# Optimization experiments

Measured on AMD Instinct MI355X. Metric: run time of the kernel, lower is better.

## Reference

```python
import jax, jax.numpy as jnp
import numpy as np

D_MODEL = 2048
D_INNER = 2048
N_QK = 32
N_V = 32
D_STATE = 64
D_CONV = 4
CHUNK = 128
CONV_DIM = D_INNER + 2 * N_QK * D_STATE  # 6144
IN_OUT = 2 * D_INNER + 2 * N_QK * D_STATE + N_V  # 8224


def setup_inputs() -> dict:
    key = jax.random.key(0)
    ks = jax.random.split(key, 6)
    u = jax.random.normal(ks[0], (2, 4096, D_MODEL), dtype=jnp.float32)
    W_in = jax.random.normal(ks[1], (IN_OUT, D_MODEL), dtype=jnp.float32) * 0.02
    conv_w = jax.random.normal(ks[2], (CONV_DIM, D_CONV), dtype=jnp.float32) * 0.2
    conv_b = jax.random.normal(ks[3], (CONV_DIM,), dtype=jnp.float32) * 0.02
    D = jnp.ones((N_V,), dtype=jnp.float32)
    z_bias = jnp.zeros((D_INNER,), dtype=jnp.float32)
    W_out = jax.random.normal(ks[4], (D_MODEL, D_INNER), dtype=jnp.float32) * 0.02
    return {"u": u, "W_in": W_in, "conv_w": conv_w, "conv_b": conv_b,
            "D": D, "z_bias": z_bias, "W_out": W_out}


def causal_depthwise_conv(x, w, b):
    # x: [B, L, C]; w: [C, K]; b: [C]. Torch Conv1d(groups=C, padding=K-1)[..., :L]
    B, L, C = x.shape
    K = w.shape[1]
    xp = jnp.pad(x, ((0, 0), (K - 1, 0), (0, 0)))
    y = b[None, None, :]
    for k in range(K):
        y = y + xp[:, k:k + L, :] * w[None, None, :, k]
    return y


def ssd_chunk_scan(x, dt, B, C, chunk):
    # Mamba2 SSD with A = -1 per head.
    # x: [b,l,h,p], dt: [b,l,h] (positive), B,C: [b,l,h,n]
    b, l, h, p = x.shape
    n = B.shape[-1]
    nc = l // chunk
    x = x.reshape(b, nc, chunk, h, p)
    dt = dt.reshape(b, nc, chunk, h)
    B = B.reshape(b, nc, chunk, h, n)
    C = C.reshape(b, nc, chunk, h, n)
    a = -dt                                  # A * dt
    cum = jnp.cumsum(a, axis=2)              # [b,nc,q,h]
    xdt = x * dt[..., None]                  # dt_t * x_t
    # ---- intra-chunk (causal, decay exp(cum_q - cum_k), q >= k) ----
    CB = jnp.einsum('bcqhn,bckhn->bchqk', C, B)
    cumT = jnp.swapaxes(cum, 2, 3)           # [b,nc,h,q]
    diff = cumT[..., :, None] - cumT[..., None, :]   # [b,nc,h,q,k]
    mask = jnp.tril(jnp.ones((chunk, chunk), dtype=bool))
    decay = jnp.exp(jnp.where(mask, diff, -jnp.inf))
    y_intra = jnp.einsum('bchqk,bckhp->bcqhp', CB * decay, xdt)
    # ---- per-chunk final states ----
    state_decay = jnp.exp(cum[:, :, -1:, :] - cum)   # [b,nc,q,h]
    states = jnp.einsum('bckhn,bckhp->bchpn', B * state_decay[..., None], xdt)
    chunk_decay = jnp.exp(cum[:, :, -1, :])          # [b,nc,h]
    # ---- inter-chunk recurrence ----
    def step(carry, inp):
        st, cd = inp  # st [b,h,p,n], cd [b,h]
        new = carry * cd[:, :, None, None] + st
        return new, carry  # emit the state *entering* this chunk
    init = jnp.zeros((b, h, p, n), dtype=x.dtype)
    _, prev = jax.lax.scan(step, init,
                           (jnp.moveaxis(states, 1, 0), jnp.moveaxis(chunk_decay, 1, 0)))
    prev = jnp.moveaxis(prev, 0, 1)                  # [b,nc,h,p,n]
    y_inter = jnp.einsum('bcqhn,bchpn->bcqhp', C * jnp.exp(cum)[..., None], prev)
    return (y_intra + y_inter).reshape(b, l, h, p)


def reference(u, W_in, conv_w, conv_b, D, z_bias, W_out):
    b, l, _ = u.shape  # l divisible by CHUNK (padded_len == l)
    xBCzA = jnp.einsum('bld,od->blo', u, W_in)
    xBC = xBCzA[..., :CONV_DIM]
    z = xBCzA[..., CONV_DIM:CONV_DIM + D_INNER]
    A_log = xBCzA[..., CONV_DIM + D_INNER:]
    xBC = causal_depthwise_conv(xBC, conv_w, conv_b)  # activation = identity
    x = xBC[..., :D_INNER]
    Bm = xBC[..., D_INNER:D_INNER + N_QK * D_STATE]
    Cm = xBC[..., D_INNER + N_QK * D_STATE:]
    x = x.reshape(b, l, N_V, D_INNER // N_V)
    Bm = Bm.reshape(b, l, N_QK, D_STATE)
    Cm = Cm.reshape(b, l, N_QK, D_STATE)
    dt = jax.nn.softplus(A_log)                       # [b,l,h]
    x_scan = x / dt[..., None]
    y = ssd_chunk_scan(x_scan, dt, Bm, Cm, CHUNK)
    y = y + D[None, None, :, None] * x                # Du uses undivided x
    y = y.reshape(b, l, D_INNER)
    out = jnp.einsum('bli,oi->blo', y * jax.nn.silu(z + z_bias), W_out)
    return out
```

## Files before the change

kernel.cpp:

```cpp
#include <hip/hip_runtime.h>
#include <math.h>

#define D_MODEL  2048
#define D_INNER  2048
#define N_QK     32
#define N_V      32
#define D_STATE  64
#define D_CONV   4
#define CHUNK    128
#define CONV_DIM 6144
#define IN_OUT   8224
#define BATCH    2
#define SEQ      4096
#define M_ROWS   (BATCH*SEQ)
#define NCHUNK   (SEQ/CHUNK)

typedef unsigned short bf16_t;
typedef __attribute__((ext_vector_type(4))) float f32x4;
typedef __attribute__((ext_vector_type(8))) short bf16x8;

#define SWZ64(r,c)  ((((r)*64)  + (c)) ^ (((r)&7)<<3))
#define SWZ128(r,c) ((((r)*128) + (c)) ^ (((r)&7)<<3))

__device__ __forceinline__ float b2f(bf16_t u) {
    union { unsigned int i; float f; } w; w.i = ((unsigned int)u) << 16; return w.f;
}
__device__ __forceinline__ bf16_t f2b(float f) {
    unsigned int x = __float_as_uint(f);
    return (bf16_t)((x + 0x7FFFu + ((x >> 16) & 1u)) >> 16);
}
__device__ __forceinline__ void store4b(bf16_t* dst, float4 v) {
    ushort4 u; u.x = f2b(v.x); u.y = f2b(v.y); u.z = f2b(v.z); u.w = f2b(v.w);
    *reinterpret_cast<ushort4*>(dst) = u;
}

__device__ __forceinline__ void gload_lds16(const bf16_t* g, bf16_t* l) {
    __builtin_amdgcn_global_load_lds((const __attribute__((address_space(1))) void*)g,
                                     (__attribute__((address_space(3))) void*)l,
                                     16, 0, 0);
}

__global__ __launch_bounds__(256) void f2b_kernel(const float* __restrict__ in,
                                                  bf16_t* __restrict__ out, long n)
{
    const long i = ((long)blockIdx.x * 256 + threadIdx.x) * 4;
    if (i < n) {
        float4 v = *reinterpret_cast<const float4*>(in + i);
        ushort4 o;
        o.x = f2b(v.x); o.y = f2b(v.y); o.z = f2b(v.z); o.w = f2b(v.w);
        *reinterpret_cast<ushort4*>(out + i) = o;
    }
}

template<int NTB, int K, bool OBF16, int NCOLS>
__global__ __launch_bounds__(512, 2) void gemm256(const bf16_t* __restrict__ A,
                                                  const bf16_t* __restrict__ B,
                                                  void* __restrict__ Cv)
{
    constexpr int BK = 64;
    constexpr int NT = K / BK;
    constexpr bool HASTAIL = (NTB * 256 > NCOLS);
    const long ldc = NCOLS;
    __shared__ bf16_t As[2][256 * BK];
    __shared__ bf16_t Bs[2][256 * BK];

    const int nwg = gridDim.x;
    const int bid = blockIdx.x;
    const int wg  = ((nwg & 7) == 0) ? ((bid & 7) * (nwg >> 3) + (bid >> 3)) : bid;
    const int bm = (wg / NTB) * 256;
    const int bn = (wg % NTB) * 256;

    const int tid  = threadIdx.x;
    const int lane = tid & 63;
    const int wv   = tid >> 6;
    const int wr   = wv >> 2, wc = wv & 3;
    const int l15  = lane & 15, l4 = lane >> 4;

    f32x4 acc[8][4];
    #pragma unroll
    for (int i = 0; i < 8; ++i)
        #pragma unroll
        for (int j = 0; j < 4; ++j) acc[i][j] = (f32x4){0.f, 0.f, 0.f, 0.f};

    const bf16_t* Abase = A + (long)bm * K;

    auto stage = [&](int t, int buf) {
        const bf16_t* Ab = Abase + t * BK;
        #pragma unroll
        for (int it = 0; it < 4; ++it) {
            const int seg = it * 512 + tid;
            const int row = seg >> 3, c16 = seg & 7;
            const int sc = (c16 ^ (row & 7)) * 8;
            gload_lds16(Ab + (long)row * K + sc, &As[buf][seg * 8]);
            int br = bn + row;
            if (HASTAIL) br = min(br, NCOLS - 1);
            gload_lds16(B + (long)br * K + t * BK + sc, &Bs[buf][seg * 8]);
        }
    };

    stage(0, 0);
    asm volatile("s_waitcnt vmcnt(0)" ::: "memory");
    __builtin_amdgcn_s_barrier();

    for (int t = 0; t < NT; ++t) {
        const int cur = t & 1;
        if (t + 1 < NT) stage(t + 1, cur ^ 1);
        bf16x8 bfr[4], af[4];
        #pragma unroll
        for (int ks = 0; ks < 2; ++ks) {
            #pragma unroll
            for (int ni = 0; ni < 4; ++ni) {
                const int row = wc * 64 + ni * 16 + l15;
                const int ch = (ks * 4 + l4) ^ (row & 7);
                bfr[ni] = *reinterpret_cast<const bf16x8*>(&Bs[cur][row * 64 + ch * 8]);
            }
            #pragma unroll
            for (int qm = 0; qm < 2; ++qm) {
                #pragma unroll
                for (int mi = 0; mi < 4; ++mi) {
                    const int row = wr * 128 + qm * 64 + mi * 16 + l15;
                    const int ch = (ks * 4 + l4) ^ (row & 7);
                    af[mi] = *reinterpret_cast<const bf16x8*>(&As[cur][row * 64 + ch * 8]);
                }
                __builtin_amdgcn_s_setprio(1);
                #pragma unroll
                for (int mi = 0; mi < 4; ++mi)
                    #pragma unroll
                    for (int ni = 0; ni < 4; ++ni)
                        acc[qm * 4 + mi][ni] = __builtin_amdgcn_mfma_f32_16x16x32_bf16(
                            af[mi], bfr[ni], acc[qm * 4 + mi][ni], 0, 0, 0);
                __builtin_amdgcn_s_setprio(0);
                if (ks * 2 + qm < 3) __builtin_amdgcn_s_barrier();
            }
        }
        asm volatile("s_waitcnt vmcnt(0)" ::: "memory");
        __builtin_amdgcn_s_barrier();
    }

    #pragma unroll
    for (int mf = 0; mf < 8; ++mf) {
        const long grow0 = bm + wr * 128 + mf * 16 + l4 * 4;
        #pragma unroll
        for (int ni = 0; ni < 4; ++ni) {
            const int gcol = bn + wc * 64 + ni * 16 + l15;
            if (HASTAIL && gcol >= NCOLS) continue;
            #pragma unroll
            for (int j = 0; j < 4; ++j) {
                if (OBF16)
                    ((bf16_t*)Cv)[(grow0 + j) * ldc + gcol] = f2b(acc[mf][ni][j]);
                else
                    ((float*)Cv)[(grow0 + j) * ldc + gcol] = acc[mf][ni][j];
            }
        }
    }
}

__device__ __forceinline__ float4 conv4v(const bf16_t* __restrict__ xb, long m, int l,
                                         int col, const float* __restrict__ cw,
                                         const float* __restrict__ cbv)
{
    float4 acc = *reinterpret_cast<const float4*>(cbv + col);
    float4 wc0 = *reinterpret_cast<const float4*>(cw + (long)col * 4);
    float4 wc1 = *reinterpret_cast<const float4*>(cw + (long)col * 4 + 4);
    float4 wc2 = *reinterpret_cast<const float4*>(cw + (long)col * 4 + 8);
    float4 wc3 = *reinterpret_cast<const float4*>(cw + (long)col * 4 + 12);
    const float t0[4] = {wc0.x, wc0.y, wc0.z, wc0.w};
    const float t1[4] = {wc1.x, wc1.y, wc1.z, wc1.w};
    const float t2[4] = {wc2.x, wc2.y, wc2.z, wc2.w};
    const float t3[4] = {wc3.x, wc3.y, wc3.z, wc3.w};
    #pragma unroll
    for (int tap = 0; tap < 4; ++tap) {
        if (l - 3 + tap < 0) continue;
        const bf16_t* p = xb + (m - 3 + tap) * (long)IN_OUT + col;
        ushort4 v = *reinterpret_cast<const ushort4*>(p);
        acc.x = fmaf(b2f(v.x), t0[tap], acc.x);
        acc.y = fmaf(b2f(v.y), t1[tap], acc.y);
        acc.z = fmaf(b2f(v.z), t2[tap], acc.z);
        acc.w = fmaf(b2f(v.w), t3[tap], acc.w);
    }
    return acc;
}

__global__ __launch_bounds__(256) void ssd_states(const bf16_t* __restrict__ xb,
                                                  const float* __restrict__ cw,
                                                  const float* __restrict__ cbv,
                                                  float* __restrict__ states,
                                                  float* __restrict__ cumbuf,
                                                  float* __restrict__ cdecay)
{
    const int h = blockIdx.x, c = blockIdx.y, b = blockIdx.z;
    __shared__ bf16_t sx [128 * 64];
    __shared__ bf16_t sBr[128 * 64];
    __shared__ bf16_t sXT[64 * 128];
    __shared__ bf16_t sBT[64 * 128];
    __shared__ float  cum[CHUNK];
    const int t = threadIdx.x;
    const long mbase = (long)b * SEQ + (long)c * CHUNK;
    const long cb = ((long)b * NCHUNK + c) * N_QK + h;

    if (t < CHUNK) {
        const float a = b2f(xb[(mbase + t) * (long)IN_OUT + (CONV_DIM + D_INNER) + h]);
        cum[t] = -((a > 20.f) ? a : log1pf(expf(a)));
    }
    for (int idx = t; idx < CHUNK * 16; idx += 256) {
        const int k = idx >> 4, q4 = (idx & 15) * 4;
        const long m = mbase + k;
        const int l = (int)(m & (SEQ - 1));
        float4 xv = conv4v(xb, m, l, h * 64 + q4, cw, cbv);
        float4 bv = conv4v(xb, m, l, D_INNER + h * 64 + q4, cw, cbv);
        store4b(&sx [SWZ64(k, q4)], xv);
        store4b(&sBr[SWZ64(k, q4)], bv);
    }
    __syncthreads();
    #pragma unroll
    for (int s = 1; s < CHUNK; s <<= 1) {
        float pv = 0.f;
        if (t < CHUNK && t >= s) pv = cum[t - s];
        __syncthreads();
        if (t < CHUNK && t >= s) cum[t] += pv;
        __syncthreads();
    }
    const float clast = cum[CHUNK - 1];
    {
        const int j = t & 127;
        const int c8b = (t >> 7) * 4;
        const float ej = __expf(clast - cum[j]);
        #pragma unroll
        for (int it = 0; it < 4; ++it) {
            const int c8 = c8b + it;
            bf16x8 xv = *reinterpret_cast<const bf16x8*>(&sx [SWZ64(j, c8 * 8)]);
            bf16x8 bv = *reinterpret_cast<const bf16x8*>(&sBr[SWZ64(j, c8 * 8)]);
            #pragma unroll
            for (int e = 0; e < 8; ++e) {
                sXT[SWZ128(c8 * 8 + e, j)] = xv[e];
                sBT[SWZ128(c8 * 8 + e, j)] = f2b(b2f((bf16_t)bv[e]) * ej);
            }
        }
    }
    __syncthreads();

    const int lane = t & 63, wv = t >> 6;
    const int l15 = lane & 15, l4 = lane >> 4;
    f32x4 acc[4];
    #pragma unroll
    for (int nj = 0; nj < 4; ++nj) acc[nj] = (f32x4){0.f, 0.f, 0.f, 0.f};
    #pragma unroll
    for (int ks = 0; ks < 4; ++ks) {
        const int kc = ks * 32 + l4 * 8;
        bf16x8 af = *reinterpret_cast<const bf16x8*>(&sXT[SWZ128(wv * 16 + l15, kc)]);
        #pragma unroll
        for (int nj = 0; nj < 4; ++nj) {
            bf16x8 bf = *reinterpret_cast<const bf16x8*>(&sBT[SWZ128(nj * 16 + l15, kc)]);
            acc[nj] = __builtin_amdgcn_mfma_f32_16x16x32_bf16(af, bf, acc[nj], 0, 0, 0);
        }
    }
    #pragma unroll
    for (int nj = 0; nj < 4; ++nj) {
        #pragma unroll
        for (int jj = 0; jj < 4; ++jj) {
            const int p = wv * 16 + l4 * 4 + jj;
            states[cb * 4096 + (long)p * 64 + nj * 16 + l15] = acc[nj][jj];
        }
    }
    if (t < CHUNK) cumbuf[cb * CHUNK + t] = cum[t];
    if (t == 0)   cdecay[cb] = __expf(clast);
}

__global__ __launch_bounds__(256) void ssd_scan(float* __restrict__ states,
                                                const float* __restrict__ cdecay)
{
    const int bid = blockIdx.x;
    const int bh = bid >> 2, q = bid & 3;
    const int b = bh >> 5, h = bh & 31;
    const int t = threadIdx.x;
    const int off = q * 1024 + t * 4;
    float4 carry = make_float4(0.f, 0.f, 0.f, 0.f);
    for (int c = 0; c < NCHUNK; ++c) {
        const long cb = ((long)b * NCHUNK + c) * N_QK + h;
        const long base = cb * 4096 + off;
        const float cd = cdecay[cb];
        float4 st = *reinterpret_cast<const float4*>(&states[base]);
        *reinterpret_cast<float4*>(&states[base]) = carry;
        carry.x = fmaf(carry.x, cd, st.x);
        carry.y = fmaf(carry.y, cd, st.y);
        carry.z = fmaf(carry.z, cd, st.z);
        carry.w = fmaf(carry.w, cd, st.w);
    }
}

__global__ __launch_bounds__(256) void ssd_out(const bf16_t* __restrict__ xb,
                                               const float* __restrict__ cumbuf,
                                               const float* __restrict__ prevst,
                                               const float* __restrict__ Dvec,
                                               const float* __restrict__ zbias,
                                               const float* __restrict__ cw,
                                               const float* __restrict__ cbv,
                                               bf16_t* __restrict__ yz)
{
    const int h = blockIdx.x, c = blockIdx.y, b = blockIdx.z;
    __shared__ bf16_t sC[128 * 64];
    __shared__ bf16_t sB[128 * 64];
    __shared__ bf16_t sXQ[128 * 64];
    __shared__ bf16_t sXT[64 * 128];
    __shared__ bf16_t sP[64 * 64];
    __shared__ float  cum[CHUNK];
    const int t = threadIdx.x;
    const long mbase = (long)b * SEQ + (long)c * CHUNK;
    const long cb = ((long)b * NCHUNK + c) * N_QK + h;
    if (t < CHUNK) cum[t] = cumbuf[cb * CHUNK + t];
    for (int idx = t; idx < CHUNK * 16; idx += 256) {
        const int k = idx >> 4, q4 = (idx & 15) * 4;
        const long m = mbase + k;
        const int l = (int)(m & (SEQ - 1));
        float4 xv = conv4v(xb, m, l, h * 64 + q4, cw, cbv);
        float4 bv = conv4v(xb, m, l, D_INNER + h * 64 + q4, cw, cbv);
        float4 cv = conv4v(xb, m, l, 2 * D_INNER + h * 64 + q4, cw, cbv);
        store4b(&sXQ[SWZ64(k, q4)], xv);
        store4b(&sB [SWZ64(k, q4)], bv);
        store4b(&sC [SWZ64(k, q4)], cv);
    }
    for (int idx = t; idx < 64 * 16; idx += 256) {
        const int p = idx >> 4, q4 = (idx & 15) * 4;
        float4 v = *reinterpret_cast<const float4*>(prevst + cb * 4096 + p * 64 + q4);
        store4b(&sP[SWZ64(p, q4)], v);
    }
    __syncthreads();
    {
        const int j = t & 127;
        const int c8b = (t >> 7) * 4;
        #pragma unroll
        for (int it = 0; it < 4; ++it) {
            const int c8 = c8b + it;
            bf16x8 v = *reinterpret_cast<const bf16x8*>(&sXQ[SWZ64(j, c8 * 8)]);
            #pragma unroll
            for (int e = 0; e < 8; ++e) sXT[SWZ128(c8 * 8 + e, j)] = v[e];
        }
    }
    __syncthreads();

    const int lane = t & 63, wv = t >> 6;
    const int w32 = wv * 32, l15 = lane & 15, l4 = lane >> 4;
    bf16_t* sQ = sXQ;

    f32x4 yac[2][4], iac[2][4];
    #pragma unroll
    for (int mi = 0; mi < 2; ++mi)
        #pragma unroll
        for (int np = 0; np < 4; ++np) {
            yac[mi][np] = (f32x4){0.f, 0.f, 0.f, 0.f};
            iac[mi][np] = (f32x4){0.f, 0.f, 0.f, 0.f};
        }

    #pragma unroll
    for (int H = 0; H < 2; ++H) {
        if (H == 1 && wv < 2) break;
        const int j0 = H * 64;
        f32x4 sac[2][4];
        #pragma unroll
        for (int mi = 0; mi < 2; ++mi)
            #pragma unroll
            for (int nj = 0; nj < 4; ++nj) sac[mi][nj] = (f32x4){0.f, 0.f, 0.f, 0.f};
        #pragma unroll
        for (int kk = 0; kk < 2; ++kk) {
            const int kc = kk * 32 + l4 * 8;
            bf16x8 af0 = *reinterpret_cast<const bf16x8*>(&sC[SWZ64(w32 + l15, kc)]);
            bf16x8 af1 = *reinterpret_cast<const bf16x8*>(&sC[SWZ64(w32 + 16 + l15, kc)]);
            #pragma unroll
            for (int nj = 0; nj < 4; ++nj) {
                bf16x8 bfj = *reinterpret_cast<const bf16x8*>(&sB[SWZ64(j0 + nj * 16 + l15, kc)]);
                if (j0 + nj * 16 <= w32 + 15)
                    sac[0][nj] = __builtin_amdgcn_mfma_f32_16x16x32_bf16(af0, bfj, sac[0][nj], 0, 0, 0);
                if (j0 + nj * 16 <= w32 + 31)
                    sac[1][nj] = __builtin_amdgcn_mfma_f32_16x16x32_bf16(af1, bfj, sac[1][nj], 0, 0, 0);
            }
        }
        #pragma unroll
        for (int mi = 0; mi < 2; ++mi) {
            #pragma unroll
            for (int nj = 0; nj < 4; ++nj) {
                const int jcol = nj * 16 + l15;
                const int jg = j0 + jcol;
                #pragma unroll
                for (int jj = 0; jj < 4; ++jj) {
                    const int i = w32 + mi * 16 + l4 * 4 + jj;
                    const float q = (jg <= i) ? __expf(cum[i] - cum[jg]) * sac[mi][nj][jj] : 0.f;
                    sQ[SWZ64(i, jcol)] = f2b(q);
                }
            }
        }
        #pragma unroll
        for (int kk = 0; kk < 2; ++kk) {
            const int kc = kk * 32 + l4 * 8;
            bf16x8 qa0 = *reinterpret_cast<const bf16x8*>(&sQ[SWZ64(w32 + l15, kc)]);
            bf16x8 qa1 = *reinterpret_cast<const bf16x8*>(&sQ[SWZ64(w32 + 16 + l15, kc)]);
            #pragma unroll
            for (int np = 0; np < 4; ++np) {
                bf16x8 xf = *reinterpret_cast<const bf16x8*>(&sXT[SWZ128(np * 16 + l15, j0 + kc)]);
                yac[0][np] = __builtin_amdgcn_mfma_f32_16x16x32_bf16(qa0, xf, yac[0][np], 0, 0, 0);
                yac[1][np] = __builtin_amdgcn_mfma_f32_16x16x32_bf16(qa1, xf, yac[1][np], 0, 0, 0);
            }
        }
    }
    #pragma unroll
    for (int kk = 0; kk < 2; ++kk) {
        const int kc = kk * 32 + l4 * 8;
        bf16x8 cf0 = *reinterpret_cast<const bf16x8*>(&sC[SWZ64(w32 + l15, kc)]);
        bf16x8 cf1 = *reinterpret_cast<const bf16x8*>(&sC[SWZ64(w32 + 16 + l15, kc)]);
        #pragma unroll
        for (int np = 0; np < 4; ++np) {
            bf16x8 pf = *reinterpret_cast<const bf16x8*>(&sP[SWZ64(np * 16 + l15, kc)]);
            iac[0][np] = __builtin_amdgcn_mfma_f32_16x16x32_bf16(cf0, pf, iac[0][np], 0, 0, 0);
            iac[1][np] = __builtin_amdgcn_mfma_f32_16x16x32_bf16(cf1, pf, iac[1][np], 0, 0, 0);
        }
    }
    const float dh = Dvec[h];
    #pragma unroll
    for (int mi = 0; mi < 2; ++mi) {
        #pragma unroll
        for (int jj = 0; jj < 4; ++jj) {
            const int i = w32 + mi * 16 + l4 * 4 + jj;
            const float ei = __expf(cum[i]);
            const long m = mbase + i;
            const bf16_t* zr = xb + m * (long)IN_OUT + CONV_DIM + h * 64;
            bf16_t* orow = yz + m * (long)D_INNER + h * 64;
            #pragma unroll
            for (int np = 0; np < 4; ++np) {
                const int p = np * 16 + l15;
                const float xval = b2f(sXT[SWZ128(p, i)]);
                const float y = yac[mi][np][jj] + ei * iac[mi][np][jj] + dh * xval;
                const float zv = b2f(zr[p]) + zbias[h * 64 + p];
                const float s = zv / (1.f + __expf(-zv));
                orow[p] = f2b(y * s);
            }
        }
    }
}

extern "C" void kernel_launch(void* const* d_in, const int* in_sizes, int n_in,
                              void* d_out, int out_size, void* d_ws, size_t ws_size,
                              hipStream_t stream)
{
    const float* u      = (const float*)d_in[0];
    const float* W_in   = (const float*)d_in[1];
    const float* conv_w = (const float*)d_in[2];
    const float* conv_b = (const float*)d_in[3];
    const float* Dv     = (const float*)d_in[4];
    const float* z_bias = (const float*)d_in[5];
    const float* W_out  = (const float*)d_in[6];
    float* out = (float*)d_out;

    char* w = (char*)d_ws;
    bf16_t* xbcza = (bf16_t*)w;  w += (long)M_ROWS * IN_OUT * 2;
    bf16_t* wob   = (bf16_t*)w;  w += (long)2048 * 2048 * 2;
    char* ureg = w;
    bf16_t* ub  = (bf16_t*)ureg;
    bf16_t* wib = (bf16_t*)(ureg + (long)M_ROWS * D_MODEL * 2);
    bf16_t* yzb = (bf16_t*)ureg;
    float*  cumb   = (float*)(ureg + (long)M_ROWS * D_INNER * 2);
    float*  states = cumb + (long)BATCH * NCHUNK * N_QK * CHUNK;
    float*  cdec   = states + (long)BATCH * NCHUNK * N_QK * 4096;

    f2b_kernel<<<(int)(((long)M_ROWS * D_MODEL / 4 + 255) / 256), 256, 0, stream>>>(
        u, ub, (long)M_ROWS * D_MODEL);
    f2b_kernel<<<(int)(((long)IN_OUT * D_MODEL / 4 + 255) / 256), 256, 0, stream>>>(
        W_in, wib, (long)IN_OUT * D_MODEL);
    f2b_kernel<<<(int)(((long)D_MODEL * D_INNER / 4 + 255) / 256), 256, 0, stream>>>(
        W_out, wob, (long)D_MODEL * D_INNER);

    gemm256<33, D_MODEL, true, IN_OUT><<<(M_ROWS / 256) * 33, 512, 0, stream>>>(
        ub, wib, xbcza);

    ssd_states<<<dim3(N_QK, NCHUNK, BATCH), 256, 0, stream>>>(xbcza, conv_w, conv_b,
                                                              states, cumb, cdec);

    ssd_scan<<<BATCH * N_QK * 4, 256, 0, stream>>>(states, cdec);

    ssd_out<<<dim3(N_QK, NCHUNK, BATCH), 256, 0, stream>>>(xbcza, cumb, states, Dv, z_bias,
                                                           conv_w, conv_b, yzb);

    gemm256<8, D_INNER, false, D_MODEL><<<(M_ROWS / 256) * 8, 512, 0, stream>>>(
        yzb, wob, out);
}
```

Before: 837.9 us.

## Split GEMM K-tiles into halves for finer prefetch overlap, separate ragged N tail

The main 256x256 GEMM now stages each BK=64 tile as two 32-wide halves with a new XOR swizzle, issuing the next tile's loads in two pieces interleaved with MFMA work. Partial vmcnt waits replace the full drain at the end of each iteration. The in-projection's 32-column tail (8224 = 8192 + 32) is moved out of the big kernel into a separate smaller 128x128 GEMM, so the main kernel no longer carries tail clamping or wasted columns. The cost is an extra kernel launch and more barriers per K-step.

```diff
diff --git a/kernel.cpp b/kernel.cpp
--- a/kernel.cpp
+++ b/kernel.cpp
@@ -52,17 +52,16 @@
     }
 }
 
-template<int NTB, int K, bool OBF16, int NCOLS>
+template<int NTB, int K, bool OBF16>
 __global__ __launch_bounds__(512, 2) void gemm256(const bf16_t* __restrict__ A,
                                                   const bf16_t* __restrict__ B,
-                                                  void* __restrict__ Cv)
+                                                  void* __restrict__ Cv,
+                                                  long ldc)
 {
     constexpr int BK = 64;
     constexpr int NT = K / BK;
-    constexpr bool HASTAIL = (NTB * 256 > NCOLS);
-    const long ldc = NCOLS;
-    __shared__ bf16_t As[2][256 * BK];
-    __shared__ bf16_t Bs[2][256 * BK];
+    __shared__ bf16_t As[2][2][8192];
+    __shared__ bf16_t Bs[2][2][8192];
 
     const int nwg = gridDim.x;
     const int bid = blockIdx.x;
@@ -83,57 +82,92 @@
         for (int j = 0; j < 4; ++j) acc[i][j] = (f32x4){0.f, 0.f, 0.f, 0.f};
 
     const bf16_t* Abase = A + (long)bm * K;
-
-    auto stage = [&](int t, int buf) {
-        const bf16_t* Ab = Abase + t * BK;
-        #pragma unroll
-        for (int it = 0; it < 4; ++it) {
-            const int seg = it * 512 + tid;
-            const int row = seg >> 3, c16 = seg & 7;
-            const int sc = (c16 ^ (row & 7)) * 8;
-            gload_lds16(Ab + (long)row * K + sc, &As[buf][seg * 8]);
-            int br = bn + row;
-            if (HASTAIL) br = min(br, NCOLS - 1);
-            gload_lds16(B + (long)br * K + t * BK + sc, &Bs[buf][seg * 8]);
+    const bf16_t* Bbase = B + (long)bn * K;
+
+    auto stage_half = [&](int t, int buf, int kh) {
+        #pragma unroll
+        for (int it = 0; it < 2; ++it) {
+            const int s   = it * 512 + tid;
+            const int row = s >> 2;
+            const int jp  = s & 3;
+            const int jl  = jp ^ ((row >> 1) & 3);
+            const long go = (long)row * K + t * BK + kh * 32 + jl * 8;
+            gload_lds16(Abase + go, &As[buf][kh][s * 8]);
+            gload_lds16(Bbase + go, &Bs[buf][kh][s * 8]);
         }
     };
-
-    stage(0, 0);
-    asm volatile("s_waitcnt vmcnt(0)" ::: "memory");
+    auto rdA = [&](int buf, int kh, int row) {
+        const int jp = l4 ^ ((row >> 1) & 3);
+        return *reinterpret_cast<const bf16x8*>(&As[buf][kh][(row * 4 + jp) * 8]);
+    };
+    auto rdB = [&](int buf, int kh, int row) {
+        const int jp = l4 ^ ((row >> 1) & 3);
+        return *reinterpret_cast<const bf16x8*>(&Bs[buf][kh][(row * 4 + jp) * 8]);
+    };
+
+    stage_half(0, 0, 0);
+    stage_half(0, 0, 1);
+    asm volatile("s_waitcnt vmcnt(4)" ::: "memory");
     __builtin_amdgcn_s_barrier();
 
     for (int t = 0; t < NT; ++t) {
         const int cur = t & 1;
-        if (t + 1 < NT) stage(t + 1, cur ^ 1);
         bf16x8 bfr[4], af[4];
-        #pragma unroll
-        for (int ks = 0; ks < 2; ++ks) {
-            #pragma unroll
-            for (int ni = 0; ni < 4; ++ni) {
-                const int row = wc * 64 + ni * 16 + l15;
-                const int ch = (ks * 4 + l4) ^ (row & 7);
-                bfr[ni] = *reinterpret_cast<const bf16x8*>(&Bs[cur][row * 64 + ch * 8]);
-            }
-            #pragma unroll
-            for (int qm = 0; qm < 2; ++qm) {
-                #pragma unroll
-                for (int mi = 0; mi < 4; ++mi) {
-                    const int row = wr * 128 + qm * 64 + mi * 16 + l15;
-                    const int ch = (ks * 4 + l4) ^ (row & 7);
-                    af[mi] = *reinterpret_cast<const bf16x8*>(&As[cur][row * 64 + ch * 8]);
-                }
-                __builtin_amdgcn_s_setprio(1);
-                #pragma unroll
-                for (int mi = 0; mi < 4; ++mi)
-                    #pragma unroll
-                    for (int ni = 0; ni < 4; ++ni)
-                        acc[qm * 4 + mi][ni] = __builtin_amdgcn_mfma_f32_16x16x32_bf16(
-                            af[mi], bfr[ni], acc[qm * 4 + mi][ni], 0, 0, 0);
-                __builtin_amdgcn_s_setprio(0);
-                if (ks * 2 + qm < 3) __builtin_amdgcn_s_barrier();
-            }
-        }
-        asm volatile("s_waitcnt vmcnt(0)" ::: "memory");
+        if (t + 1 < NT) stage_half(t + 1, cur ^ 1, 0);
+        #pragma unroll
+        for (int ni = 0; ni < 4; ++ni) bfr[ni] = rdB(cur, 0, wc * 64 + ni * 16 + l15);
+        #pragma unroll
+        for (int mi = 0; mi < 4; ++mi) af[mi] = rdA(cur, 0, wr * 128 + mi * 16 + l15);
+        __builtin_amdgcn_s_setprio(1);
+        #pragma unroll
+        for (int mi = 0; mi < 4; ++mi)
+            #pragma unroll
+            for (int ni = 0; ni < 4; ++ni)
+                acc[mi][ni] = __builtin_amdgcn_mfma_f32_16x16x32_bf16(
+                    af[mi], bfr[ni], acc[mi][ni], 0, 0, 0);
+        __builtin_amdgcn_s_setprio(0);
+        __builtin_amdgcn_s_barrier();
+        #pragma unroll
+        for (int mi = 0; mi < 4; ++mi) af[mi] = rdA(cur, 0, wr * 128 + 64 + mi * 16 + l15);
+        __builtin_amdgcn_s_setprio(1);
+        #pragma unroll
+        for (int mi = 0; mi < 4; ++mi)
+            #pragma unroll
+            for (int ni = 0; ni < 4; ++ni)
+                acc[4 + mi][ni] = __builtin_amdgcn_mfma_f32_16x16x32_bf16(
+                    af[mi], bfr[ni], acc[4 + mi][ni], 0, 0, 0);
+        __builtin_amdgcn_s_setprio(0);
+        if (t + 1 < NT) {
+            stage_half(t + 1, cur ^ 1, 1);
+            asm volatile("s_waitcnt vmcnt(8)" ::: "memory");
+        } else {
+            asm volatile("s_waitcnt vmcnt(0)" ::: "memory");
+        }
+        __builtin_amdgcn_s_barrier();
+        #pragma unroll
+        for (int ni = 0; ni < 4; ++ni) bfr[ni] = rdB(cur, 1, wc * 64 + ni * 16 + l15);
+        #pragma unroll
+        for (int mi = 0; mi < 4; ++mi) af[mi] = rdA(cur, 1, wr * 128 + mi * 16 + l15);
+        __builtin_amdgcn_s_setprio(1);
+        #pragma unroll
+        for (int mi = 0; mi < 4; ++mi)
+            #pragma unroll
+            for (int ni = 0; ni < 4; ++ni)
+                acc[mi][ni] = __builtin_amdgcn_mfma_f32_16x16x32_bf16(
+                    af[mi], bfr[ni], acc[mi][ni], 0, 0, 0);
+        __builtin_amdgcn_s_setprio(0);
+        __builtin_amdgcn_s_barrier();
+        #pragma unroll
+        for (int mi = 0; mi < 4; ++mi) af[mi] = rdA(cur, 1, wr * 128 + 64 + mi * 16 + l15);
+        __builtin_amdgcn_s_setprio(1);
+        #pragma unroll
+        for (int mi = 0; mi < 4; ++mi)
+            #pragma unroll
+            for (int ni = 0; ni < 4; ++ni)
+                acc[4 + mi][ni] = __builtin_amdgcn_mfma_f32_16x16x32_bf16(
+                    af[mi], bfr[ni], acc[4 + mi][ni], 0, 0, 0);
+        __builtin_amdgcn_s_setprio(0);
+        if (t + 1 < NT) { asm volatile("s_waitcnt vmcnt(4)" ::: "memory"); }
         __builtin_amdgcn_s_barrier();
     }
 
@@ -143,13 +177,95 @@
         #pragma unroll
         for (int ni = 0; ni < 4; ++ni) {
             const int gcol = bn + wc * 64 + ni * 16 + l15;
-            if (HASTAIL && gcol >= NCOLS) continue;
             #pragma unroll
             for (int j = 0; j < 4; ++j) {
                 if (OBF16)
                     ((bf16_t*)Cv)[(grow0 + j) * ldc + gcol] = f2b(acc[mf][ni][j]);
                 else
                     ((float*)Cv)[(grow0 + j) * ldc + gcol] = acc[mf][ni][j];
+            }
+        }
+    }
+}
+
+template<int N, int K, bool OBF16>
+__global__ __launch_bounds__(256) void gemm_mfma(const bf16_t* __restrict__ A,
+                                                 const bf16_t* __restrict__ B,
+                                                 void* __restrict__ Cv,
+                                                 long ldc)
+{
+    constexpr int BM = 128, BN = 128, BK = 64;
+    constexpr int NTB = (N + BN - 1) / BN;
+    __shared__ bf16_t As[BM * BK];
+    __shared__ bf16_t Bs[BM * BK];
+
+    const int nwg = gridDim.x;
+    const int bid = blockIdx.x;
+    const int wg  = ((nwg & 7) == 0) ? ((bid & 7) * (nwg >> 3) + (bid >> 3)) : bid;
+    const int bm = (wg / NTB) * BM;
+    const int bn = (wg % NTB) * BN;
+
+    const int tid  = threadIdx.x;
+    const int lane = tid & 63;
+    const int wv   = tid >> 6;
+    const int wr   = wv >> 1, wc = wv & 1;
+
+    f32x4 acc[4][4];
+    #pragma unroll
+    for (int i = 0; i < 4; ++i)
+        #pragma unroll
+        for (int j = 0; j < 4; ++j) acc[i][j] = (f32x4){0.f, 0.f, 0.f, 0.f};
+
+    for (int k0 = 0; k0 < K; k0 += BK) {
+        #pragma unroll
+        for (int it = 0; it < 4; ++it) {
+            const int seg = it * 256 + tid;
+            const int row = seg >> 3, c16 = seg & 7;
+            gload_lds16(A + (long)(bm + row) * K + k0 + c16 * 8,
+                        &As[row * BK + c16 * 8]);
+            int brow = bn + row;
+            if constexpr (N % BN != 0) brow = min(brow, N - 1);
+            gload_lds16(B + (long)brow * K + k0 + c16 * 8,
+                        &Bs[row * BK + c16 * 8]);
+        }
+        __syncthreads();
+        #pragma unroll
+        for (int kk = 0; kk < 2; ++kk) {
+            bf16x8 af[4], bfr[4];
+            const int kc = kk * 32 + (lane >> 4) * 8;
+            #pragma unroll
+            for (int mi = 0; mi < 4; ++mi) {
+                const int row = wr * 64 + mi * 16 + (lane & 15);
+                af[mi] = *reinterpret_cast<const bf16x8*>(&As[row * BK + kc]);
+            }
+            #pragma unroll
+            for (int ni = 0; ni < 4; ++ni) {
+                const int row = wc * 64 + ni * 16 + (lane & 15);
+                bfr[ni] = *reinterpret_cast<const bf16x8*>(&Bs[row * BK + kc]);
+            }
+            #pragma unroll
+            for (int mi = 0; mi < 4; ++mi)
+                #pragma unroll
+                for (int ni = 0; ni < 4; ++ni)
+                    acc[mi][ni] = __builtin_amdgcn_mfma_f32_16x16x32_bf16(
+                        af[mi], bfr[ni], acc[mi][ni], 0, 0, 0);
+        }
+        __syncthreads();
+    }
+
+    #pragma unroll
+    for (int mi = 0; mi < 4; ++mi) {
+        const long row0 = bm + wr * 64 + mi * 16 + ((lane >> 4) << 2);
+        #pragma unroll
+        for (int ni = 0; ni < 4; ++ni) {
+            const int col = bn + wc * 64 + ni * 16 + (lane & 15);
+            if (N % BN != 0 && col >= N) continue;
+            #pragma unroll
+            for (int j = 0; j < 4; ++j) {
+                if (OBF16)
+                    ((bf16_t*)Cv)[(row0 + j) * ldc + col] = f2b(acc[mi][ni][j]);
+                else
+                    ((float*)Cv)[(row0 + j) * ldc + col] = acc[mi][ni][j];
             }
         }
     }
@@ -467,8 +583,10 @@
     f2b_kernel<<<(int)(((long)D_MODEL * D_INNER / 4 + 255) / 256), 256, 0, stream>>>(
         W_out, wob, (long)D_MODEL * D_INNER);
 
-    gemm256<33, D_MODEL, true, IN_OUT><<<(M_ROWS / 256) * 33, 512, 0, stream>>>(
-        ub, wib, xbcza);
+    gemm256<32, D_MODEL, true><<<(M_ROWS / 256) * 32, 512, 0, stream>>>(
+        ub, wib, xbcza, IN_OUT);
+    gemm_mfma<32, D_MODEL, true><<<(M_ROWS / 128), 256, 0, stream>>>(
+        ub, wib + (long)8192 * D_MODEL, xbcza + 8192, IN_OUT);
 
     ssd_states<<<dim3(N_QK, NCHUNK, BATCH), 256, 0, stream>>>(xbcza, conv_w, conv_b,
                                                               states, cumb, cdec);
@@ -478,6 +596,6 @@
     ssd_out<<<dim3(N_QK, NCHUNK, BATCH), 256, 0, stream>>>(xbcza, cumb, states, Dv, z_bias,
                                                            conv_w, conv_b, yzb);
 
-    gemm256<8, D_INNER, false, D_MODEL><<<(M_ROWS / 256) * 8, 512, 0, stream>>>(
-        yzb, wob, out);
-}
+    gemm256<8, D_INNER, false><<<(M_ROWS / 256) * 8, 512, 0, stream>>>(
+        yzb, wob, out, D_MODEL);
+}
```

Measured after the change: 830.6 us. Within noise of the previous version (-0.9%).
